# Kernel tuning notes

Measured on AMD Instinct MI355X. Metric: run time of the kernel, lower is better.

The kernel has to match this reference:

```python
import jax, jax.numpy as jnp
import numpy as np

EPS = 1e-12  # matches torch F.normalize default eps


def _normalize(x):
    n = jnp.linalg.norm(x, axis=-1, keepdims=True)
    return x / jnp.maximum(n, EPS)


def _time_interp(t, e, L, E):
    """linear_interpolation_time: [B] t,e; L:[m] landmarks; E:[m,m] emb table."""
    m = L.shape[0]
    idx = jnp.searchsorted(L, t)              # torch.searchsorted, side='left'
    idx = jnp.where(idx == 0, 1, idx)
    idx = jnp.where(idx == m, m - 1, idx)
    E_hi, E_lo = E[idx], E[idx - 1]           # [B, m]
    L_hi, L_lo = L[idx], L[idx - 1]           # [B]
    coef = (E_hi - E_lo) / (L_hi - L_lo)[:, None]
    out = E_lo + coef * (t - L_lo)[:, None]
    # censor mask row i: mean of landmark embeddings j >= idx[i]
    denom = (m - idx).astype(E.dtype)[:, None]
    mask = (jnp.arange(m)[None, :] >= idx[:, None]).astype(E.dtype) / denom  # [B, m]
    out_censor = mask @ E.T                   # [B, m]
    e = e[:, None]
    return (out * e + out_censor * (1.0 - e)).astype(jnp.float32)


def setup_inputs() -> dict:
    key = jax.random.key(0)
    B, m = 8192, 256
    k_z, k_t, k_e = jax.random.split(key, 3)
    z = jax.random.normal(k_z, (B, m), dtype=jnp.float32)
    t = jax.random.uniform(k_t, (B,), dtype=jnp.float32, minval=0.0, maxval=10.0)
    e = (jax.random.uniform(k_e, (B,)) < 0.7).astype(jnp.float32)
    log_tau = jnp.zeros((1,), dtype=jnp.float32)            # tau=1.0 -> log 1 = 0
    time_landmark = jnp.linspace(0.0, 10.0, m, dtype=jnp.float32)
    time_emb_landmark = jnp.eye(m, dtype=jnp.float32)        # learnable eye init
    return {"z": z, "t": t, "e": e, "log_tau": log_tau,
            "time_emb_landmark": time_emb_landmark, "time_landmark": time_landmark}


def reference(z, t, e, log_tau, time_emb_landmark, time_landmark):
    B = z.shape[0]
    tau = jnp.sqrt(jnp.exp(log_tau))                         # [1]
    hz = _normalize(z) / tau                                  # enc = Identity
    hy = _normalize(_time_interp(t, e, time_landmark, time_emb_landmark)) / tau
    sim = hz @ hy.T                                           # [B, B]
    g = jnp.diagonal(sim)[:, None]                            # positives [B,1]
    # off-diagonal logits g0 - g: mask diagonal with -inf (exp -> 0 in logsumexp)
    eye = jnp.eye(B, dtype=bool)
    logits = jnp.where(eye, -jnp.inf, sim - g)
    slogits = jax.nn.logsumexp(logits, axis=1, keepdims=True)  # [B,1]
    # CrossEntropyLoss(sim, arange) per row = logsumexp(sim) - sim[i,i]
    dummy_ce = (jax.nn.logsumexp(sim, axis=1, keepdims=True) - g) - jnp.log(
        jnp.float32(B))
    out = jax.lax.stop_gradient(dummy_ce) + jnp.exp(
        slogits - jax.lax.stop_gradient(slogits)) - 1.0
    return jnp.clip(out, -5.0, 15.0)                          # [B,1]
```

## Files before the change

### kernel.cpp

```cpp
#include <hip/hip_runtime.h>
#include <hip/hip_bf16.h>

using short8 = __attribute__((ext_vector_type(8))) short;
using f32x4  = __attribute__((ext_vector_type(4))) float;

#define BM 256
#define BN 256
#define BK 64
#define NKT 4

__device__ inline void gload_lds16(const void* g, void* lds) {
    __builtin_amdgcn_global_load_lds(
        (const __attribute__((address_space(1))) void*)g,
        (__attribute__((address_space(3))) void*)lds, 16, 0, 0);
}

__global__ __launch_bounds__(256) void suffix_kernel(const float* __restrict__ E,
                                                     float* __restrict__ ST, int m) {
    int j = blockIdx.x;
    int k = threadIdx.x;
    int lane = k & 63, w = k >> 6;
    __shared__ float wtot[4];
    float v = (k < m) ? E[(size_t)j * m + k] : 0.f;
    #pragma unroll
    for (int off = 1; off < 64; off <<= 1) {
        float o = __shfl_down(v, off);
        if (lane + off < 64) v += o;
    }
    if (lane == 0) wtot[w] = v;
    __syncthreads();
    float add = 0.f;
    #pragma unroll
    for (int w2 = 0; w2 < 4; ++w2)
        if (w2 > w) add += wtot[w2];
    v += add;
    if (k < m) ST[(size_t)k * m + j] = v;
}

__global__ __launch_bounds__(256) void prep_kernel(
    const float* __restrict__ z, const float* __restrict__ t,
    const float* __restrict__ e, const float* __restrict__ log_tau,
    const float* __restrict__ E, const float* __restrict__ L,
    const float* __restrict__ ST,
    __hip_bfloat16* __restrict__ hz, __hip_bfloat16* __restrict__ hy,
    float* __restrict__ g, float* __restrict__ acc, int B, int m)
{
    int row  = blockIdx.x * 4 + (threadIdx.x >> 6);
    int lane = threadIdx.x & 63;
    if (row >= B) return;

    float tv = t[row], ev = e[row];

    int lo = 0, hi = m;
    while (lo < hi) { int mid = (lo + hi) >> 1; if (L[mid] < tv) lo = mid + 1; else hi = mid; }
    int idx = lo;
    if (idx == 0) idx = 1;
    if (idx == m) idx = m - 1;

    float Llo = L[idx - 1], Lhi = L[idx];
    float w    = (tv - Llo) / (Lhi - Llo);
    float invd = 1.0f / (float)(m - idx);
    float tau  = sqrtf(expf(log_tau[0]));
    float invtau = 1.0f / tau;

    int j0 = lane * 4;
    f32x4 zz = *(const f32x4*)&z[(size_t)row * m + j0];
    f32x4 El = *(const f32x4*)&E[(size_t)(idx - 1) * m + j0];
    f32x4 Eh = *(const f32x4*)&E[(size_t)idx * m + j0];
    f32x4 Sc = *(const f32x4*)&ST[(size_t)idx * m + j0];

    float yv[4];
    float ssy = 0.f, ssz = 0.f;
    #pragma unroll
    for (int p = 0; p < 4; ++p) {
        float yint = El[p] + (Eh[p] - El[p]) * w;
        float ycen = Sc[p] * invd;
        float y = yint * ev + ycen * (1.f - ev);
        yv[p] = y; ssy += y * y;
        ssz += zz[p] * zz[p];
    }
    #pragma unroll
    for (int off = 1; off < 64; off <<= 1) {
        ssy += __shfl_xor(ssy, off);
        ssz += __shfl_xor(ssz, off);
    }
    float sy = invtau / fmaxf(sqrtf(ssy), 1e-12f);
    float sz = invtau / fmaxf(sqrtf(ssz), 1e-12f);

    float gp = 0.f;
    ushort uy[4], uz[4];
    #pragma unroll
    for (int p = 0; p < 4; ++p) {
        float hyv = yv[p] * sy, hzv = zz[p] * sz;
        gp += hyv * hzv;
        __hip_bfloat16 hb = __float2bfloat16(hyv);
        __hip_bfloat16 zb = __float2bfloat16(hzv);
        uy[p] = *reinterpret_cast<unsigned short*>(&hb);
        uz[p] = *reinterpret_cast<unsigned short*>(&zb);
    }
    *(ushort4*)&hy[(size_t)row * m + j0] = make_ushort4(uy[0], uy[1], uy[2], uy[3]);
    *(ushort4*)&hz[(size_t)row * m + j0] = make_ushort4(uz[0], uz[1], uz[2], uz[3]);
    #pragma unroll
    for (int off = 1; off < 64; off <<= 1) gp += __shfl_xor(gp, off);
    if (lane == 0) { g[row] = gp; acc[row] = 0.f; }
}

__global__ __launch_bounds__(512, 2) void gemm_lse_kernel(
    const __hip_bfloat16* __restrict__ hz, const __hip_bfloat16* __restrict__ hy,
    float* __restrict__ row_acc, int Brows, int K)
{
    __shared__ __hip_bfloat16 As[2][BM * BK];
    __shared__ __hip_bfloat16 Bs[2][BN * BK];

    const int tid  = threadIdx.x;
    const int wid  = tid >> 6;
    const int lane = tid & 63;
    const int wm   = wid >> 2;
    const int wn   = wid & 3;

    int bx = blockIdx.x, by = blockIdx.y;
    if (gridDim.x == 32 && gridDim.y == 32) {
        int orig = by * 32 + bx;
        int xcd = orig & 7, pos = orig >> 3;
        by = (xcd << 2) | (pos & 3);
        bx = pos >> 2;
    }
    const int row0 = by * BM, col0 = bx * BN;

    f32x4 acc[8][4];
    #pragma unroll
    for (int i = 0; i < 8; ++i)
        #pragma unroll
        for (int j = 0; j < 4; ++j)
            acc[i][j] = (f32x4){0.f, 0.f, 0.f, 0.f};

    const int srow = tid >> 3;
    const int c8   = tid & 7;
    const int cg   = c8 ^ (srow & 7);
    const int lm   = lane & 15, lk = lane >> 4;

#define STAGE_A(buf, kt)                                                        \
    do {                                                                        \
        _Pragma("unroll")                                                       \
        for (int s = 0; s < 4; ++s)                                             \
            gload_lds16(hz + (size_t)(row0 + s * 64 + srow) * K + (kt) * BK + cg * 8, \
                        (void*)&As[buf][s * 4096 + wid * 512]);                 \
    } while (0)
#define STAGE_B(buf, kt)                                                        \
    do {                                                                        \
        _Pragma("unroll")                                                       \
        for (int s = 0; s < 4; ++s)                                             \
            gload_lds16(hy + (size_t)(col0 + s * 64 + srow) * K + (kt) * BK + cg * 8, \
                        (void*)&Bs[buf][s * 4096 + wid * 512]);                 \
    } while (0)

#define LDSA(buf, rt, q) (*(const short8*)&As[buf][(rt) * BK + ((q) ^ ((rt) & 7)) * 8])
#define LDSB(buf, rt, q) (*(const short8*)&Bs[buf][(rt) * BK + ((q) ^ ((rt) & 7)) * 8])

    STAGE_A(0, 0);
    STAGE_B(0, 0);
    asm volatile("s_waitcnt vmcnt(0)" ::: "memory");
    __builtin_amdgcn_s_barrier();

    #pragma unroll
    for (int kt = 0; kt < NKT; ++kt) {
        const int cur = kt & 1, nxt = cur ^ 1;
        short8 a[4], b[4];

        #pragma unroll
        for (int mi = 0; mi < 4; ++mi)
            a[mi] = LDSA(cur, wm * 128 + mi * 16 + lm, lk);
        #pragma unroll
        for (int ni = 0; ni < 4; ++ni)
            b[ni] = LDSB(cur, wn * 64 + ni * 16 + lm, lk);
        if (kt + 1 < NKT) STAGE_A(nxt, kt + 1);
        __builtin_amdgcn_s_barrier();
        __builtin_amdgcn_s_setprio(1);
        #pragma unroll
        for (int mi = 0; mi < 4; ++mi)
            #pragma unroll
            for (int ni = 0; ni < 4; ++ni)
                acc[mi][ni] = __builtin_amdgcn_mfma_f32_16x16x32_bf16(a[mi], b[ni], acc[mi][ni], 0, 0, 0);
        __builtin_amdgcn_s_setprio(0);
        __builtin_amdgcn_s_barrier();

        #pragma unroll
        for (int mi = 0; mi < 4; ++mi)
            a[mi] = LDSA(cur, wm * 128 + 64 + mi * 16 + lm, lk);
        if (kt + 1 < NKT) STAGE_B(nxt, kt + 1);
        __builtin_amdgcn_s_barrier();
        __builtin_amdgcn_s_setprio(1);
        #pragma unroll
        for (int mi = 0; mi < 4; ++mi)
            #pragma unroll
            for (int ni = 0; ni < 4; ++ni)
                acc[4 + mi][ni] = __builtin_amdgcn_mfma_f32_16x16x32_bf16(a[mi], b[ni], acc[4 + mi][ni], 0, 0, 0);
        __builtin_amdgcn_s_setprio(0);
        __builtin_amdgcn_s_barrier();

        #pragma unroll
        for (int mi = 0; mi < 4; ++mi)
            a[mi] = LDSA(cur, wm * 128 + mi * 16 + lm, 4 + lk);
        #pragma unroll
        for (int ni = 0; ni < 4; ++ni)
            b[ni] = LDSB(cur, wn * 64 + ni * 16 + lm, 4 + lk);
        __builtin_amdgcn_s_barrier();
        __builtin_amdgcn_s_setprio(1);
        #pragma unroll
        for (int mi = 0; mi < 4; ++mi)
            #pragma unroll
            for (int ni = 0; ni < 4; ++ni)
                acc[mi][ni] = __builtin_amdgcn_mfma_f32_16x16x32_bf16(a[mi], b[ni], acc[mi][ni], 0, 0, 0);
        __builtin_amdgcn_s_setprio(0);
        __builtin_amdgcn_s_barrier();

        #pragma unroll
        for (int mi = 0; mi < 4; ++mi)
            a[mi] = LDSA(cur, wm * 128 + 64 + mi * 16 + lm, 4 + lk);
        __builtin_amdgcn_s_barrier();
        __builtin_amdgcn_s_setprio(1);
        #pragma unroll
        for (int mi = 0; mi < 4; ++mi)
            #pragma unroll
            for (int ni = 0; ni < 4; ++ni)
                acc[4 + mi][ni] = __builtin_amdgcn_mfma_f32_16x16x32_bf16(a[mi], b[ni], acc[4 + mi][ni], 0, 0, 0);
        __builtin_amdgcn_s_setprio(0);
        asm volatile("s_waitcnt vmcnt(0)" ::: "memory");
        __builtin_amdgcn_s_barrier();
    }
#undef STAGE_A
#undef STAGE_B
#undef LDSA
#undef LDSB

    const int lg = lane >> 4;
    #pragma unroll
    for (int mi = 0; mi < 8; ++mi) {
        float rs[4] = {0.f, 0.f, 0.f, 0.f};
        #pragma unroll
        for (int ni = 0; ni < 4; ++ni) {
            #pragma unroll
            for (int r = 0; r < 4; ++r) rs[r] += __expf(acc[mi][ni][r]);
        }
        #pragma unroll
        for (int r = 0; r < 4; ++r) {
            float s = rs[r];
            s += __shfl_xor(s, 1);
            s += __shfl_xor(s, 2);
            s += __shfl_xor(s, 4);
            s += __shfl_xor(s, 8);
            if (lm == 0)
                unsafeAtomicAdd(&row_acc[row0 + wm * 128 + mi * 16 + lg * 4 + r], s);
        }
    }
}

__global__ void finalize_kernel(const float* __restrict__ acc, const float* __restrict__ g,
                                float* __restrict__ out, int B) {
    int i = blockIdx.x * 256 + threadIdx.x;
    if (i < B) {
        float v = logf(acc[i]) - g[i] - logf((float)B);
        out[i] = fminf(fmaxf(v, -5.f), 15.f);
    }
}

extern "C" void kernel_launch(void* const* d_in, const int* in_sizes, int n_in,
                              void* d_out, int out_size, void* d_ws, size_t ws_size,
                              hipStream_t stream) {
    const float* z       = (const float*)d_in[0];
    const float* t       = (const float*)d_in[1];
    const float* e       = (const float*)d_in[2];
    const float* log_tau = (const float*)d_in[3];
    const float* E       = (const float*)d_in[4];
    const float* L       = (const float*)d_in[5];
    float* out = (float*)d_out;

    const int B = in_sizes[1];
    const int m = in_sizes[5];

    char* w = (char*)d_ws;
    __hip_bfloat16* hz = (__hip_bfloat16*)w;
    __hip_bfloat16* hy = hz + (size_t)B * m;
    float* ST  = (float*)(hy + (size_t)B * m);
    float* g   = ST + (size_t)m * m;
    float* acc = g + B;

    suffix_kernel<<<m, 256, 0, stream>>>(E, ST, m);
    prep_kernel<<<B / 4, 256, 0, stream>>>(z, t, e, log_tau, E, L, ST, hz, hy, g, acc, B, m);
    dim3 grid2(B / BN, B / BM);
    gemm_lse_kernel<<<grid2, 512, 0, stream>>>(hz, hy, acc, B, m);
    finalize_kernel<<<(B + 255) / 256, 256, 0, stream>>>(acc, g, out, B);
}
```

Before: 135.1 us.

## Prefetch two K tiles, fold finalize into GEMM, widen prep rows per block

The GEMM main loop is restructured to stage two K tiles ahead and use counted vmcnt waits instead of full drains, with fewer barriers per tile. The finalize kernel is removed: the last GEMM block, detected through an atomic completion counter, computes the log, subtracts and clamps. Prep now handles 16 rows per block with 16 lanes per row and wider vector stores. The aim is to hide global-load latency and cut one kernel launch, at the cost of a serial tail in the last block and subtle wait-count correctness.

```diff
diff --git a/kernel.cpp b/kernel.cpp
--- a/kernel.cpp
+++ b/kernel.cpp
@@ -1,8 +1,9 @@
 #include <hip/hip_runtime.h>
 #include <hip/hip_bf16.h>
 
-using short8 = __attribute__((ext_vector_type(8))) short;
-using f32x4  = __attribute__((ext_vector_type(4))) float;
+using short8  = __attribute__((ext_vector_type(8))) short;
+using ushort8 = __attribute__((ext_vector_type(8))) unsigned short;
+using f32x4   = __attribute__((ext_vector_type(4))) float;
 
 #define BM 256
 #define BN 256
@@ -43,11 +44,13 @@
     const float* __restrict__ E, const float* __restrict__ L,
     const float* __restrict__ ST,
     __hip_bfloat16* __restrict__ hz, __hip_bfloat16* __restrict__ hy,
-    float* __restrict__ g, float* __restrict__ acc, int B, int m)
+    float* __restrict__ g, float* __restrict__ acc, unsigned* __restrict__ done,
+    int B, int m)
 {
-    int row  = blockIdx.x * 4 + (threadIdx.x >> 6);
-    int lane = threadIdx.x & 63;
-    if (row >= B) return;
+    const int tid = threadIdx.x;
+    const int row = blockIdx.x * 16 + (tid >> 4);
+    const int sub = tid & 15;
+    if (blockIdx.x == 0 && tid == 0) *done = 0u;
 
     float tv = t[row], ev = e[row];
 
@@ -60,27 +63,30 @@
     float Llo = L[idx - 1], Lhi = L[idx];
     float w    = (tv - Llo) / (Lhi - Llo);
     float invd = 1.0f / (float)(m - idx);
-    float tau  = sqrtf(expf(log_tau[0]));
-    float invtau = 1.0f / tau;
-
-    int j0 = lane * 4;
-    f32x4 zz = *(const f32x4*)&z[(size_t)row * m + j0];
-    f32x4 El = *(const f32x4*)&E[(size_t)(idx - 1) * m + j0];
-    f32x4 Eh = *(const f32x4*)&E[(size_t)idx * m + j0];
-    f32x4 Sc = *(const f32x4*)&ST[(size_t)idx * m + j0];
-
-    float yv[4];
+    float invtau = expf(-0.5f * log_tau[0]);
+
+    const int j0 = sub * 16;
+    f32x4 zv[4], El4[4], Eh4[4], Sc4[4], yv[4];
+    #pragma unroll
+    for (int q = 0; q < 4; ++q) {
+        zv[q]  = *(const f32x4*)&z [(size_t)row * m + j0 + q * 4];
+        El4[q] = *(const f32x4*)&E [(size_t)(idx - 1) * m + j0 + q * 4];
+        Eh4[q] = *(const f32x4*)&E [(size_t)idx * m + j0 + q * 4];
+        Sc4[q] = *(const f32x4*)&ST[(size_t)idx * m + j0 + q * 4];
+    }
     float ssy = 0.f, ssz = 0.f;
     #pragma unroll
-    for (int p = 0; p < 4; ++p) {
-        float yint = El[p] + (Eh[p] - El[p]) * w;
-        float ycen = Sc[p] * invd;
-        float y = yint * ev + ycen * (1.f - ev);
-        yv[p] = y; ssy += y * y;
-        ssz += zz[p] * zz[p];
-    }
-    #pragma unroll
-    for (int off = 1; off < 64; off <<= 1) {
+    for (int q = 0; q < 4; ++q)
+        #pragma unroll
+        for (int p = 0; p < 4; ++p) {
+            float yint = El4[q][p] + (Eh4[q][p] - El4[q][p]) * w;
+            float ycen = Sc4[q][p] * invd;
+            float y = yint * ev + ycen * (1.f - ev);
+            yv[q][p] = y; ssy += y * y;
+            ssz += zv[q][p] * zv[q][p];
+        }
+    #pragma unroll
+    for (int off = 1; off < 16; off <<= 1) {
         ssy += __shfl_xor(ssy, off);
         ssz += __shfl_xor(ssz, off);
     }
@@ -88,26 +94,31 @@
     float sz = invtau / fmaxf(sqrtf(ssz), 1e-12f);
 
     float gp = 0.f;
-    ushort uy[4], uz[4];
-    #pragma unroll
-    for (int p = 0; p < 4; ++p) {
-        float hyv = yv[p] * sy, hzv = zz[p] * sz;
-        gp += hyv * hzv;
-        __hip_bfloat16 hb = __float2bfloat16(hyv);
-        __hip_bfloat16 zb = __float2bfloat16(hzv);
-        uy[p] = *reinterpret_cast<unsigned short*>(&hb);
-        uz[p] = *reinterpret_cast<unsigned short*>(&zb);
-    }
-    *(ushort4*)&hy[(size_t)row * m + j0] = make_ushort4(uy[0], uy[1], uy[2], uy[3]);
-    *(ushort4*)&hz[(size_t)row * m + j0] = make_ushort4(uz[0], uz[1], uz[2], uz[3]);
-    #pragma unroll
-    for (int off = 1; off < 64; off <<= 1) gp += __shfl_xor(gp, off);
-    if (lane == 0) { g[row] = gp; acc[row] = 0.f; }
+    ushort8 oy[2], oz[2];
+    #pragma unroll
+    for (int q = 0; q < 4; ++q)
+        #pragma unroll
+        for (int p = 0; p < 4; ++p) {
+            float hyv = yv[q][p] * sy, hzv = zv[q][p] * sz;
+            gp += hyv * hzv;
+            __hip_bfloat16 hb = __float2bfloat16(hyv);
+            __hip_bfloat16 zb = __float2bfloat16(hzv);
+            oy[q >> 1][(q & 1) * 4 + p] = *reinterpret_cast<unsigned short*>(&hb);
+            oz[q >> 1][(q & 1) * 4 + p] = *reinterpret_cast<unsigned short*>(&zb);
+        }
+    *(ushort8*)&hy[(size_t)row * m + j0]     = oy[0];
+    *(ushort8*)&hy[(size_t)row * m + j0 + 8] = oy[1];
+    *(ushort8*)&hz[(size_t)row * m + j0]     = oz[0];
+    *(ushort8*)&hz[(size_t)row * m + j0 + 8] = oz[1];
+    #pragma unroll
+    for (int off = 1; off < 16; off <<= 1) gp += __shfl_xor(gp, off);
+    if (sub == 0) { g[row] = gp; acc[row] = 0.f; }
 }
 
 __global__ __launch_bounds__(512, 2) void gemm_lse_kernel(
     const __hip_bfloat16* __restrict__ hz, const __hip_bfloat16* __restrict__ hy,
-    float* __restrict__ row_acc, int Brows, int K)
+    float* __restrict__ row_acc, const float* __restrict__ gvec,
+    float* __restrict__ out, unsigned* __restrict__ done, int Brows, int K)
 {
     __shared__ __hip_bfloat16 As[2][BM * BK];
     __shared__ __hip_bfloat16 Bs[2][BN * BK];
@@ -139,99 +150,82 @@
     const int cg   = c8 ^ (srow & 7);
     const int lm   = lane & 15, lk = lane >> 4;
 
-#define STAGE_A(buf, kt)                                                        \
-    do {                                                                        \
-        _Pragma("unroll")                                                       \
-        for (int s = 0; s < 4; ++s)                                             \
+#define STAGE_B(buf, kt)                                                          \
+    do {                                                                          \
+        _Pragma("unroll")                                                         \
+        for (int s = 0; s < 4; ++s)                                               \
+            gload_lds16(hy + (size_t)(col0 + s * 64 + srow) * K + (kt) * BK + cg * 8, \
+                        (void*)&Bs[buf][s * 4096 + wid * 512]);                   \
+    } while (0)
+#define STAGE_A(buf, kt)                                                          \
+    do {                                                                          \
+        const int sord[4] = {0, 2, 1, 3};                                         \
+        _Pragma("unroll")                                                         \
+        for (int si = 0; si < 4; ++si) {                                          \
+            int s = sord[si];                                                     \
             gload_lds16(hz + (size_t)(row0 + s * 64 + srow) * K + (kt) * BK + cg * 8, \
-                        (void*)&As[buf][s * 4096 + wid * 512]);                 \
-    } while (0)
-#define STAGE_B(buf, kt)                                                        \
-    do {                                                                        \
-        _Pragma("unroll")                                                       \
-        for (int s = 0; s < 4; ++s)                                             \
-            gload_lds16(hy + (size_t)(col0 + s * 64 + srow) * K + (kt) * BK + cg * 8, \
-                        (void*)&Bs[buf][s * 4096 + wid * 512]);                 \
+                        (void*)&As[buf][s * 4096 + wid * 512]);                   \
+        }                                                                         \
     } while (0)
 
 #define LDSA(buf, rt, q) (*(const short8*)&As[buf][(rt) * BK + ((q) ^ ((rt) & 7)) * 8])
 #define LDSB(buf, rt, q) (*(const short8*)&Bs[buf][(rt) * BK + ((q) ^ ((rt) & 7)) * 8])
 
+    short8 a[4], b[4];
+#define RD_A(CUR, HALF, KB)                                                       \
+    { _Pragma("unroll")                                                           \
+      for (int mi = 0; mi < 4; ++mi)                                              \
+          a[mi] = LDSA(CUR, wm * 128 + (HALF) * 64 + mi * 16 + lm, (KB) + lk); }
+#define RD_B(CUR, KB)                                                             \
+    { _Pragma("unroll")                                                           \
+      for (int ni = 0; ni < 4; ++ni)                                              \
+          b[ni] = LDSB(CUR, wn * 64 + ni * 16 + lm, (KB) + lk); }
+#define MM(BASE)                                                                  \
+    { __builtin_amdgcn_s_setprio(1);                                              \
+      _Pragma("unroll")                                                           \
+      for (int mi = 0; mi < 4; ++mi)                                              \
+          _Pragma("unroll")                                                       \
+          for (int ni = 0; ni < 4; ++ni)                                          \
+              acc[(BASE) + mi][ni] = __builtin_amdgcn_mfma_f32_16x16x32_bf16(     \
+                  a[mi], b[ni], acc[(BASE) + mi][ni], 0, 0, 0);                   \
+      __builtin_amdgcn_s_setprio(0); }
+
+#define FENCE asm volatile("" ::: "memory")
+
+#define TILE(CUR, NXT, DO_STAGE, KT, W0S, W1S)                                    \
+    {                                                                             \
+        if (DO_STAGE) STAGE_B(NXT, (KT) + 1);                                     \
+        asm volatile("s_waitcnt vmcnt(" W0S ")" ::: "memory");                    \
+        __builtin_amdgcn_s_barrier(); FENCE;                                      \
+        RD_A(CUR, 0, 0) RD_B(CUR, 0) MM(0)                                        \
+        if (DO_STAGE) STAGE_A(NXT, (KT) + 1);                                     \
+        asm volatile("s_waitcnt vmcnt(" W1S ")" ::: "memory");                    \
+        __builtin_amdgcn_s_barrier(); FENCE;                                      \
+        RD_A(CUR, 1, 0) MM(4)                                                     \
+        RD_A(CUR, 0, 4) RD_B(CUR, 4) MM(0)                                        \
+        RD_A(CUR, 1, 4) MM(4)                                                     \
+        asm volatile("s_waitcnt lgkmcnt(0)" ::: "memory");                        \
+        __builtin_amdgcn_s_barrier(); FENCE;                                      \
+    }
+
+    STAGE_B(0, 0);
     STAGE_A(0, 0);
-    STAGE_B(0, 0);
-    asm volatile("s_waitcnt vmcnt(0)" ::: "memory");
-    __builtin_amdgcn_s_barrier();
-
-    #pragma unroll
-    for (int kt = 0; kt < NKT; ++kt) {
-        const int cur = kt & 1, nxt = cur ^ 1;
-        short8 a[4], b[4];
-
-        #pragma unroll
-        for (int mi = 0; mi < 4; ++mi)
-            a[mi] = LDSA(cur, wm * 128 + mi * 16 + lm, lk);
-        #pragma unroll
-        for (int ni = 0; ni < 4; ++ni)
-            b[ni] = LDSB(cur, wn * 64 + ni * 16 + lm, lk);
-        if (kt + 1 < NKT) STAGE_A(nxt, kt + 1);
-        __builtin_amdgcn_s_barrier();
-        __builtin_amdgcn_s_setprio(1);
-        #pragma unroll
-        for (int mi = 0; mi < 4; ++mi)
-            #pragma unroll
-            for (int ni = 0; ni < 4; ++ni)
-                acc[mi][ni] = __builtin_amdgcn_mfma_f32_16x16x32_bf16(a[mi], b[ni], acc[mi][ni], 0, 0, 0);
-        __builtin_amdgcn_s_setprio(0);
-        __builtin_amdgcn_s_barrier();
-
-        #pragma unroll
-        for (int mi = 0; mi < 4; ++mi)
-            a[mi] = LDSA(cur, wm * 128 + 64 + mi * 16 + lm, lk);
-        if (kt + 1 < NKT) STAGE_B(nxt, kt + 1);
-        __builtin_amdgcn_s_barrier();
-        __builtin_amdgcn_s_setprio(1);
-        #pragma unroll
-        for (int mi = 0; mi < 4; ++mi)
-            #pragma unroll
-            for (int ni = 0; ni < 4; ++ni)
-                acc[4 + mi][ni] = __builtin_amdgcn_mfma_f32_16x16x32_bf16(a[mi], b[ni], acc[4 + mi][ni], 0, 0, 0);
-        __builtin_amdgcn_s_setprio(0);
-        __builtin_amdgcn_s_barrier();
-
-        #pragma unroll
-        for (int mi = 0; mi < 4; ++mi)
-            a[mi] = LDSA(cur, wm * 128 + mi * 16 + lm, 4 + lk);
-        #pragma unroll
-        for (int ni = 0; ni < 4; ++ni)
-            b[ni] = LDSB(cur, wn * 64 + ni * 16 + lm, 4 + lk);
-        __builtin_amdgcn_s_barrier();
-        __builtin_amdgcn_s_setprio(1);
-        #pragma unroll
-        for (int mi = 0; mi < 4; ++mi)
-            #pragma unroll
-            for (int ni = 0; ni < 4; ++ni)
-                acc[mi][ni] = __builtin_amdgcn_mfma_f32_16x16x32_bf16(a[mi], b[ni], acc[mi][ni], 0, 0, 0);
-        __builtin_amdgcn_s_setprio(0);
-        __builtin_amdgcn_s_barrier();
-
-        #pragma unroll
-        for (int mi = 0; mi < 4; ++mi)
-            a[mi] = LDSA(cur, wm * 128 + 64 + mi * 16 + lm, 4 + lk);
-        __builtin_amdgcn_s_barrier();
-        __builtin_amdgcn_s_setprio(1);
-        #pragma unroll
-        for (int mi = 0; mi < 4; ++mi)
-            #pragma unroll
-            for (int ni = 0; ni < 4; ++ni)
-                acc[4 + mi][ni] = __builtin_amdgcn_mfma_f32_16x16x32_bf16(a[mi], b[ni], acc[4 + mi][ni], 0, 0, 0);
-        __builtin_amdgcn_s_setprio(0);
-        asm volatile("s_waitcnt vmcnt(0)" ::: "memory");
-        __builtin_amdgcn_s_barrier();
-    }
+    STAGE_B(1, 1);
+    STAGE_A(1, 1);
+
+    TILE(0, 1, 0, 0, "10", "8")
+    TILE(1, 0, 1, 1, "6",  "8")
+    TILE(0, 1, 1, 2, "6",  "8")
+    TILE(1, 0, 0, 3, "2",  "0")
+
+#undef TILE
 #undef STAGE_A
 #undef STAGE_B
 #undef LDSA
 #undef LDSB
+#undef RD_A
+#undef RD_B
+#undef MM
 
     const int lg = lane >> 4;
     #pragma unroll
@@ -253,14 +247,23 @@
                 unsafeAtomicAdd(&row_acc[row0 + wm * 128 + mi * 16 + lg * 4 + r], s);
         }
     }
-}
-
-__global__ void finalize_kernel(const float* __restrict__ acc, const float* __restrict__ g,
-                                float* __restrict__ out, int B) {
-    int i = blockIdx.x * 256 + threadIdx.x;
-    if (i < B) {
-        float v = logf(acc[i]) - g[i] - logf((float)B);
-        out[i] = fminf(fmaxf(v, -5.f), 15.f);
+
+    __threadfence();
+    __shared__ unsigned islast;
+    if (tid == 0) {
+        unsigned old = atomicAdd(done, 1u);
+        islast = (old == gridDim.x * gridDim.y - 1) ? 1u : 0u;
+    }
+    __syncthreads();
+    if (islast) {
+        __threadfence();
+        const float lb = logf((float)Brows);
+        for (int i = tid; i < Brows; i += 512) {
+            float av = __hip_atomic_load(&row_acc[i], __ATOMIC_RELAXED,
+                                         __HIP_MEMORY_SCOPE_AGENT);
+            float v = logf(av) - gvec[i] - lb;
+            out[i] = fminf(fmaxf(v, -5.f), 15.f);
+        }
     }
 }
 
@@ -281,13 +284,13 @@
     char* w = (char*)d_ws;
     __hip_bfloat16* hz = (__hip_bfloat16*)w;
     __hip_bfloat16* hy = hz + (size_t)B * m;
-    float* ST  = (float*)(hy + (size_t)B * m);
-    float* g   = ST + (size_t)m * m;
-    float* acc = g + B;
+    float* ST   = (float*)(hy + (size_t)B * m);
+    float* g    = ST + (size_t)m * m;
+    float* acc  = g + B;
+    unsigned* done = (unsigned*)(acc + B);
 
     suffix_kernel<<<m, 256, 0, stream>>>(E, ST, m);
-    prep_kernel<<<B / 4, 256, 0, stream>>>(z, t, e, log_tau, E, L, ST, hz, hy, g, acc, B, m);
+    prep_kernel<<<B / 16, 256, 0, stream>>>(z, t, e, log_tau, E, L, ST, hz, hy, g, acc, done, B, m);
     dim3 grid2(B / BN, B / BM);
-    gemm_lse_kernel<<<grid2, 512, 0, stream>>>(hz, hy, acc, B, m);
-    finalize_kernel<<<(B + 255) / 256, 256, 0, stream>>>(acc, g, out, B);
-}
+    gemm_lse_kernel<<<grid2, 512, 0, stream>>>(hz, hy, acc, g, out, done, B, m);
+}
```

After: 246.8 us. +82.7%, slower.
